# Performance work log

Hardware: AMD Instinct MI355X
Metric: run time of the kernel (lower is better)

Reference implementation:

```python
import jax, jax.numpy as jnp
import numpy as np

N_ATOMS = 6144
BOX = 40.0  # Angstrom, simulation box edge


def setup_inputs() -> dict:
    key = jax.random.key(0)
    k1, k2 = jax.random.split(key)
    coordinates = jax.random.uniform(k1, (1, N_ATOMS, 3), dtype=jnp.float32) * BOX
    species = jax.random.randint(k2, (1, N_ATOMS), 0, 4)  # no -1 dummy atoms
    return {"species": species, "coordinates": coordinates, "cutoff": 5}


def reference(species, coordinates, cutoff):
    # Faithful math of CellList.forward with pbc=None (no PBC):
    # the grid/bucket pipeline only accelerates finding all (i, j), i > j
    # pairs with |r_i - r_j| <= cutoff (tril_indices ordering), excluding
    # dummy atoms (species == -1). Output: dense masked distance map where
    # entry [i, j] = distance if pair is a screened neighbor else 0.
    coords = coordinates.reshape(-1, 3)
    n = coords.shape[0]
    cutoff = jnp.float32(cutoff)
    diff = coords[:, None, :] - coords[None, :, :]           # [N, N, 3] = r_i - r_j
    sq = jnp.sum(diff * diff, axis=-1)                       # [N, N]
    dist = jnp.sqrt(jnp.where(sq > 0, sq, 1.0))              # safe sqrt (diag sq==0)
    dummy = species.reshape(-1) == -1
    valid = jnp.tril(jnp.ones((n, n), dtype=bool), k=-1)     # i > j, as tril_indices(offset=-1)
    valid = valid & (~dummy[:, None]) & (~dummy[None, :])
    # screening uses detached coords in the original -> mask is non-diff anyway
    mask = valid & (dist <= cutoff) & (sq > 0)
    return jnp.where(mask, dist, 0.0)
```

## Files before the change

kernel.cpp:

```cpp
#include <hip/hip_runtime.h>
#include <math.h>


constexpr int N      = 6144;
constexpr int BLOCK  = 256;
constexpr int CPB    = 2048;
constexpr int HALF   = CPB / 2;
constexpr int NSTRIP = N / CPB;
constexpr int RPB    = 6;
constexpr int NROWG  = N / RPB;

__global__ __launch_bounds__(BLOCK) void cell_list_kernel(
    const float* __restrict__ coords,
    const int*   __restrict__ species,
    const int*   __restrict__ cutoff_p,
    float*       __restrict__ out)
{
    const int bx    = blockIdx.x;
    const int strip = bx % NSTRIP;
    const int i0    = (bx / NSTRIP) * RPB;
    const int base  = strip * CPB;
    const int jA    = base + (int)threadIdx.x * 4;
    const int jB    = jA + HALF;

    const float  c  = (float)cutoff_p[0];
    const float  cn = __int_as_float(__float_as_int(c) + 1);
    const double md = (double)c + 0.5 * ((double)cn - (double)c);
    const double Td = md * md;
    float T = (float)Td;
    if ((double)T > Td) T = __int_as_float(__float_as_int(T) - 1);

    float fA[12], fB[12];
    int   sA[4],  sB[4];
    if (i0 + RPB - 1 > base) {
        const float4* ca = reinterpret_cast<const float4*>(coords + 3 * (size_t)jA);
        const float4* cb = reinterpret_cast<const float4*>(coords + 3 * (size_t)jB);
#pragma unroll
        for (int q = 0; q < 3; ++q) {
            const float4 va = ca[q];
            fA[4 * q + 0] = va.x; fA[4 * q + 1] = va.y;
            fA[4 * q + 2] = va.z; fA[4 * q + 3] = va.w;
            const float4 vb = cb[q];
            fB[4 * q + 0] = vb.x; fB[4 * q + 1] = vb.y;
            fB[4 * q + 2] = vb.z; fB[4 * q + 3] = vb.w;
        }
        const int4 sa = *reinterpret_cast<const int4*>(species + jA);
        const int4 sb = *reinterpret_cast<const int4*>(species + jB);
        sA[0] = sa.x; sA[1] = sa.y; sA[2] = sa.z; sA[3] = sa.w;
        sB[0] = sb.x; sB[1] = sb.y; sB[2] = sb.z; sB[3] = sb.w;
    }

    const float4 zero4 = make_float4(0.f, 0.f, 0.f, 0.f);

    for (int rr = 0; rr < RPB; ++rr) {
        const int i = i0 + rr;
        float4* ovA = reinterpret_cast<float4*>(out + (size_t)i * N + jA);
        float4* ovB = reinterpret_cast<float4*>(out + (size_t)i * N + jB);
        const int si = species[i];

        if (i <= base || si == -1) {
            *ovA = zero4;
            *ovB = zero4;
            continue;
        }

        const float xi = coords[3 * i + 0];
        const float yi = coords[3 * i + 1];
        const float zi = coords[3 * i + 2];

        float rA[4], rB[4];
#pragma unroll
        for (int k = 0; k < 4; ++k) {
            {
                const float dx = __fsub_rn(xi, fA[3 * k + 0]);
                const float dy = __fsub_rn(yi, fA[3 * k + 1]);
                const float dz = __fsub_rn(zi, fA[3 * k + 2]);
                const float sq = __fadd_rn(
                    __fadd_rn(__fmul_rn(dx, dx), __fmul_rn(dy, dy)),
                    __fmul_rn(dz, dz));
                const bool m = (sq <= T) && (sA[k] != -1) && (jA + k < i);
                rA[k] = m ? __builtin_amdgcn_sqrtf(sq) : 0.0f;
            }
            {
                const float dx = __fsub_rn(xi, fB[3 * k + 0]);
                const float dy = __fsub_rn(yi, fB[3 * k + 1]);
                const float dz = __fsub_rn(zi, fB[3 * k + 2]);
                const float sq = __fadd_rn(
                    __fadd_rn(__fmul_rn(dx, dx), __fmul_rn(dy, dy)),
                    __fmul_rn(dz, dz));
                const bool m = (sq <= T) && (sB[k] != -1) && (jB + k < i);
                rB[k] = m ? __builtin_amdgcn_sqrtf(sq) : 0.0f;
            }
        }
        *ovA = make_float4(rA[0], rA[1], rA[2], rA[3]);
        *ovB = make_float4(rB[0], rB[1], rB[2], rB[3]);
    }
}

extern "C" void kernel_launch(void* const* d_in, const int* in_sizes, int n_in,
                              void* d_out, int out_size, void* d_ws, size_t ws_size,
                              hipStream_t stream) {
    const int*   species = (const int*)d_in[0];
    const float* coords  = (const float*)d_in[1];
    const int*   cutoff  = (const int*)d_in[2];
    float*       out     = (float*)d_out;

    dim3 block(BLOCK);
    dim3 grid(NSTRIP * NROWG);
    hipLaunchKernelGGL(cell_list_kernel, grid, block, 0, stream,
                       coords, species, cutoff, out);
}
```

Measured before the change: 155.9 us.

## Split into bulk zero-fill kernel plus sparse scatter of in-cutoff distances

Replaces the single dense compute-and-store kernel with two launches. The first streams float4 zeros over the whole output. The second tiles lower-triangular 128x128 blocks, keeps i-coordinates in LDS, and writes only the entries that pass the cutoff. The aim is to make the dense traffic a pure streaming memset and to do sparse scalar writes for the few neighbor pairs, at the cost of an extra launch and uncoalesced scattered stores.

```diff
diff --git a/kernel.cpp b/kernel.cpp
--- a/kernel.cpp
+++ b/kernel.cpp
@@ -2,26 +2,35 @@
 #include <math.h>
 
 
-constexpr int N      = 6144;
-constexpr int BLOCK  = 256;
-constexpr int CPB    = 2048;
-constexpr int HALF   = CPB / 2;
-constexpr int NSTRIP = N / CPB;
-constexpr int RPB    = 6;
-constexpr int NROWG  = N / RPB;
+constexpr int N = 6144;
 
-__global__ __launch_bounds__(BLOCK) void cell_list_kernel(
+constexpr int ZBLOCKS = 2304;
+constexpr int ZTHREADS = 256;
+constexpr int ZTOTAL4 = N * N / 4;
+constexpr int ZPT = ZTOTAL4 / (ZBLOCKS * ZTHREADS);
+
+__global__ __launch_bounds__(ZTHREADS) void zero_kernel(float4* __restrict__ out4)
+{
+    const size_t idx = (size_t)blockIdx.x * ZTHREADS + threadIdx.x;
+    const float4 z = make_float4(0.f, 0.f, 0.f, 0.f);
+    const size_t stride = (size_t)ZBLOCKS * ZTHREADS;
+#pragma unroll
+    for (int q = 0; q < ZPT; ++q)
+        out4[idx + (size_t)q * stride] = z;
+}
+
+constexpr int TILE  = 128;
+constexpr int NT    = N / TILE;
+
+__global__ __launch_bounds__(256) void pair_kernel(
     const float* __restrict__ coords,
     const int*   __restrict__ species,
     const int*   __restrict__ cutoff_p,
     float*       __restrict__ out)
 {
-    const int bx    = blockIdx.x;
-    const int strip = bx % NSTRIP;
-    const int i0    = (bx / NSTRIP) * RPB;
-    const int base  = strip * CPB;
-    const int jA    = base + (int)threadIdx.x * 4;
-    const int jB    = jA + HALF;
+    const int tj = blockIdx.x;
+    const int ti = blockIdx.y;
+    if (ti < tj) return;
 
     const float  c  = (float)cutoff_p[0];
     const float  cn = __int_as_float(__float_as_int(c) + 1);
@@ -30,70 +39,42 @@
     float T = (float)Td;
     if ((double)T > Td) T = __int_as_float(__float_as_int(T) - 1);
 
-    float fA[12], fB[12];
-    int   sA[4],  sB[4];
-    if (i0 + RPB - 1 > base) {
-        const float4* ca = reinterpret_cast<const float4*>(coords + 3 * (size_t)jA);
-        const float4* cb = reinterpret_cast<const float4*>(coords + 3 * (size_t)jB);
-#pragma unroll
-        for (int q = 0; q < 3; ++q) {
-            const float4 va = ca[q];
-            fA[4 * q + 0] = va.x; fA[4 * q + 1] = va.y;
-            fA[4 * q + 2] = va.z; fA[4 * q + 3] = va.w;
-            const float4 vb = cb[q];
-            fB[4 * q + 0] = vb.x; fB[4 * q + 1] = vb.y;
-            fB[4 * q + 2] = vb.z; fB[4 * q + 3] = vb.w;
-        }
-        const int4 sa = *reinterpret_cast<const int4*>(species + jA);
-        const int4 sb = *reinterpret_cast<const int4*>(species + jB);
-        sA[0] = sa.x; sA[1] = sa.y; sA[2] = sa.z; sA[3] = sa.w;
-        sB[0] = sb.x; sB[1] = sb.y; sB[2] = sb.z; sB[3] = sb.w;
+    __shared__ float4 ilds[TILE];
+
+    const int t  = (int)threadIdx.x;
+    const int jl = t & (TILE - 1);
+    const int ih = t >> 7;
+
+    if (t < TILE) {
+        const int i = ti * TILE + t;
+        ilds[t] = make_float4(coords[3 * i + 0], coords[3 * i + 1],
+                              coords[3 * i + 2], __int_as_float(species[i]));
     }
 
-    const float4 zero4 = make_float4(0.f, 0.f, 0.f, 0.f);
+    const int   j  = tj * TILE + jl;
+    const float xj = coords[3 * j + 0];
+    const float yj = coords[3 * j + 1];
+    const float zj = coords[3 * j + 2];
+    const bool  jok = (species[j] != -1);
 
-    for (int rr = 0; rr < RPB; ++rr) {
-        const int i = i0 + rr;
-        float4* ovA = reinterpret_cast<float4*>(out + (size_t)i * N + jA);
-        float4* ovB = reinterpret_cast<float4*>(out + (size_t)i * N + jB);
-        const int si = species[i];
+    __syncthreads();
 
-        if (i <= base || si == -1) {
-            *ovA = zero4;
-            *ovB = zero4;
-            continue;
-        }
-
-        const float xi = coords[3 * i + 0];
-        const float yi = coords[3 * i + 1];
-        const float zi = coords[3 * i + 2];
-
-        float rA[4], rB[4];
-#pragma unroll
-        for (int k = 0; k < 4; ++k) {
-            {
-                const float dx = __fsub_rn(xi, fA[3 * k + 0]);
-                const float dy = __fsub_rn(yi, fA[3 * k + 1]);
-                const float dz = __fsub_rn(zi, fA[3 * k + 2]);
-                const float sq = __fadd_rn(
-                    __fadd_rn(__fmul_rn(dx, dx), __fmul_rn(dy, dy)),
-                    __fmul_rn(dz, dz));
-                const bool m = (sq <= T) && (sA[k] != -1) && (jA + k < i);
-                rA[k] = m ? __builtin_amdgcn_sqrtf(sq) : 0.0f;
-            }
-            {
-                const float dx = __fsub_rn(xi, fB[3 * k + 0]);
-                const float dy = __fsub_rn(yi, fB[3 * k + 1]);
-                const float dz = __fsub_rn(zi, fB[3 * k + 2]);
-                const float sq = __fadd_rn(
-                    __fadd_rn(__fmul_rn(dx, dx), __fmul_rn(dy, dy)),
-                    __fmul_rn(dz, dz));
-                const bool m = (sq <= T) && (sB[k] != -1) && (jB + k < i);
-                rB[k] = m ? __builtin_amdgcn_sqrtf(sq) : 0.0f;
-            }
-        }
-        *ovA = make_float4(rA[0], rA[1], rA[2], rA[3]);
-        *ovB = make_float4(rB[0], rB[1], rB[2], rB[3]);
+    const int il0 = ih * 64;
+#pragma unroll 4
+    for (int q = 0; q < 64; ++q) {
+        const int il = il0 + q;
+        const float4 ic = ilds[il];
+        const int    i  = ti * TILE + il;
+        const float dx = __fsub_rn(ic.x, xj);
+        const float dy = __fsub_rn(ic.y, yj);
+        const float dz = __fsub_rn(ic.z, zj);
+        const float sq = __fadd_rn(
+            __fadd_rn(__fmul_rn(dx, dx), __fmul_rn(dy, dy)),
+            __fmul_rn(dz, dz));
+        const bool m = (sq <= T) && jok &&
+                       (__float_as_int(ic.w) != -1) && (j < i);
+        if (m)
+            out[(size_t)i * N + j] = __builtin_amdgcn_sqrtf(sq);
     }
 }
 
@@ -105,8 +86,8 @@
     const int*   cutoff  = (const int*)d_in[2];
     float*       out     = (float*)d_out;
 
-    dim3 block(BLOCK);
-    dim3 grid(NSTRIP * NROWG);
-    hipLaunchKernelGGL(cell_list_kernel, grid, block, 0, stream,
+    hipLaunchKernelGGL(zero_kernel, dim3(ZBLOCKS), dim3(ZTHREADS), 0, stream,
+                       reinterpret_cast<float4*>(out));
+    hipLaunchKernelGGL(pair_kernel, dim3(NT, NT), dim3(256), 0, stream,
                        coords, species, cutoff, out);
 }
```

After: 163.6 us. 4.9% more time.
